# Optimization experiments

Measured on AMD Instinct MI355X. Metric: run time of the kernel, lower is better.

The kernel has to match this reference:

```python
import jax, jax.numpy as jnp
import numpy as np

N_ATOMS = 100000
N_EDGES = 300000
ATOM_DIM = 32
BOND_DIM = 16
STEPS = 4


def setup_inputs() -> dict:
    key = jax.random.key(0)
    ks = jax.random.split(key, 8)
    atom_features = jax.random.normal(ks[0], (N_ATOMS, ATOM_DIM), dtype=jnp.float32)
    bond_features = jax.random.normal(ks[1], (N_EDGES, BOND_DIM), dtype=jnp.float32)
    pair_indices = jax.random.randint(ks[2], (N_EDGES, 2), 0, N_ATOMS, dtype=jnp.int64 if jax.config.jax_enable_x64 else jnp.int32)
    W_bond = jax.random.normal(ks[3], (BOND_DIM, ATOM_DIM * ATOM_DIM), dtype=jnp.float32) * 0.05
    b_bond = jnp.zeros((ATOM_DIM * ATOM_DIM,), dtype=jnp.float32)
    W_ih = jax.random.normal(ks[4], (3 * ATOM_DIM, ATOM_DIM), dtype=jnp.float32) * 0.1
    W_hh = jax.random.normal(ks[5], (3 * ATOM_DIM, ATOM_DIM), dtype=jnp.float32) * 0.1
    b_ih = jnp.zeros((3 * ATOM_DIM,), dtype=jnp.float32)
    b_hh = jnp.zeros((3 * ATOM_DIM,), dtype=jnp.float32)
    return {
        'atom_features': atom_features,
        'bond_features': bond_features,
        'pair_indices': pair_indices,
        'W_bond': W_bond, 'b_bond': b_bond,
        'W_ih': W_ih, 'W_hh': W_hh, 'b_ih': b_ih, 'b_hh': b_hh,
    }


def _gru_cell(x, h, W_ih, W_hh, b_ih, b_hh):
    # torch.nn.GRUCell semantics
    gi = x @ W_ih.T + b_ih  # [N, 3H]
    gh = h @ W_hh.T + b_hh
    i_r, i_z, i_n = jnp.split(gi, 3, axis=-1)
    h_r, h_z, h_n = jnp.split(gh, 3, axis=-1)
    r = jax.nn.sigmoid(i_r + h_r)
    z = jax.nn.sigmoid(i_z + h_z)
    n = jnp.tanh(i_n + r * h_n)
    return (1.0 - z) * n + z * h


def reference(atom_features, bond_features, pair_indices, W_bond, b_bond, W_ih, W_hh, b_ih, b_hh):
    n_atoms, d = atom_features.shape
    # Edge transform matrices (identical every step in the original; hoisted)
    edge_mats = (bond_features @ W_bond + b_bond).reshape(-1, d, d)  # [E, d, d]
    dst = pair_indices[:, 0]
    nbr = pair_indices[:, 1]
    h = atom_features
    for _ in range(STEPS):
        # gather neighbor states, per-edge matvec, scatter-add
        msg = jnp.einsum('eij,ej->ei', edge_mats, h[nbr])  # [E, d]
        agg = jax.ops.segment_sum(msg, dst, num_segments=n_atoms)  # [N, d]
        h = _gru_cell(agg, h, W_ih, W_hh, b_ih, b_hh)
    return h
```

## Files before the change

kernel.cpp:

```cpp
#include <hip/hip_runtime.h>
#include <hip/hip_cooperative_groups.h>

namespace cg = cooperative_groups;

#define NA 100000
#define NE 300000
#define STEPS 4
#define NTILES (NE / 16)
#define ATILES (NA / 16)

typedef _Float16 f16;
typedef _Float16 half8 __attribute__((ext_vector_type(8)));
using f32x4 = __attribute__((ext_vector_type(4))) float;

__device__ __forceinline__ void msg_body(
    const f16* __restrict__ h, const f16* __restrict__ bondp,
    const int* __restrict__ nbrp, const f16* __restrict__ Wbt,
    f16* __restrict__ msgb, int wid, int nw, int col, int kg)
{
    half8 w0[17], w1[17];
#pragma unroll
    for (int t = 0; t < 17; ++t) {
        w0[t] = *reinterpret_cast<const half8*>(Wbt + (t * 32 + col) * 32 + kg * 8);
        w1[t] = *reinterpret_cast<const half8*>(Wbt + (t * 32 + 16 + col) * 32 + kg * 8);
    }
    int tile = wid;
    int pos = 0;
    half8 hf{}, cA{}, cB{};
    if (tile < NTILES) {
        pos = tile * 16 + col;
        int nbr0 = nbrp[pos];
        cA = *reinterpret_cast<const half8*>(bondp + (size_t)pos * 16);
        cB = *reinterpret_cast<const half8*>(bondp + (size_t)pos * 16 + 8);
        hf = *reinterpret_cast<const half8*>(h + (size_t)nbr0 * 32 + kg * 8);
    }
    while (tile < NTILES) {
        int tile2 = tile + nw;
        int pos2 = 0;
        half8 hf2{}, cA2{}, cB2{};
        if (tile2 < NTILES) {
            pos2 = tile2 * 16 + col;
            int nbr2 = nbrp[pos2];
            cA2 = *reinterpret_cast<const half8*>(bondp + (size_t)pos2 * 16);
            cB2 = *reinterpret_cast<const half8*>(bondp + (size_t)pos2 * 16 + 8);
            hf2 = *reinterpret_cast<const half8*>(h + (size_t)nbr2 * 32 + kg * 8);
        }
        f32x4 acc0 = {0.f, 0.f, 0.f, 0.f};
        f32x4 acc1 = {0.f, 0.f, 0.f, 0.f};
#pragma unroll
        for (int t = 0; t < 16; ++t) {
            f16 ch = (t < 8) ? cA[t] : cB[t - 8];
            half8 a = hf * ch;
            acc0 = __builtin_amdgcn_mfma_f32_16x16x32_f16(w0[t], a, acc0, 0, 0, 0);
            acc1 = __builtin_amdgcn_mfma_f32_16x16x32_f16(w1[t], a, acc1, 0, 0, 0);
        }
        acc0 = __builtin_amdgcn_mfma_f32_16x16x32_f16(w0[16], hf, acc0, 0, 0, 0);
        acc1 = __builtin_amdgcn_mfma_f32_16x16x32_f16(w1[16], hf, acc1, 0, 0, 0);

        half8 so;
        so[0]=(f16)acc0[0]; so[1]=(f16)acc0[1]; so[2]=(f16)acc0[2]; so[3]=(f16)acc0[3];
        so[4]=(f16)acc1[0]; so[5]=(f16)acc1[1]; so[6]=(f16)acc1[2]; so[7]=(f16)acc1[3];
        *reinterpret_cast<half8*>(msgb + (size_t)pos * 32 + kg * 8) = so;

        tile = tile2; pos = pos2; hf = hf2; cA = cA2; cB = cB2;
    }
}

__device__ __forceinline__ void gru_body(
    const f16* __restrict__ msgb, const int* __restrict__ start,
    const int* __restrict__ cnt, f16* __restrict__ h,
    const f16* __restrict__ Wihb, const f16* __restrict__ Whhb,
    const float* __restrict__ bih, const float* __restrict__ bhh,
    float* __restrict__ hout, int wf, int wid, int nw, int col, int kg)
{
    half8 wi[6], wh[6];
#pragma unroll
    for (int t = 0; t < 6; ++t) {
        wi[t] = *reinterpret_cast<const half8*>(Wihb + (size_t)(t * 16 + col) * 32 + kg * 8);
        wh[t] = *reinterpret_cast<const half8*>(Whhb + (size_t)(t * 16 + col) * 32 + kg * 8);
    }
    float br0  = bih[col]      + bhh[col];
    float bz0  = bih[32 + col] + bhh[32 + col];
    float bin0 = bih[64 + col];
    float bhn0 = bhh[64 + col];
    float br1  = bih[16 + col] + bhh[16 + col];
    float bz1  = bih[48 + col] + bhh[48 + col];
    float bin1 = bih[80 + col];
    float bhn1 = bhh[80 + col];

    for (int tile = wid; tile < ATILES; tile += nw) {
        int base = tile * 16;
        int a0   = base + col;
        int st = start[a0], en = st + cnt[a0];
        half8 hfrag = *reinterpret_cast<const half8*>(h + (size_t)a0 * 32 + kg * 8);

        float xs[8] = {0.f, 0.f, 0.f, 0.f, 0.f, 0.f, 0.f, 0.f};
        int p = st;
        while (p < en) {
            int n = en - p;
            half8 m0, m1, m2, m3;
            m0 = *reinterpret_cast<const half8*>(msgb + (size_t)p * 32 + kg * 8);
            if (n > 1) m1 = *reinterpret_cast<const half8*>(msgb + (size_t)(p + 1) * 32 + kg * 8);
            if (n > 2) m2 = *reinterpret_cast<const half8*>(msgb + (size_t)(p + 2) * 32 + kg * 8);
            if (n > 3) m3 = *reinterpret_cast<const half8*>(msgb + (size_t)(p + 3) * 32 + kg * 8);
#pragma unroll
            for (int j = 0; j < 8; ++j) xs[j] += (float)m0[j];
            if (n > 1) {
#pragma unroll
                for (int j = 0; j < 8; ++j) xs[j] += (float)m1[j];
            }
            if (n > 2) {
#pragma unroll
                for (int j = 0; j < 8; ++j) xs[j] += (float)m2[j];
            }
            if (n > 3) {
#pragma unroll
                for (int j = 0; j < 8; ++j) xs[j] += (float)m3[j];
            }
            p += 4;
        }
        half8 xfrag;
#pragma unroll
        for (int j = 0; j < 8; ++j) xfrag[j] = (f16)xs[j];

        f32x4 gi[6], gh[6];
#pragma unroll
        for (int t = 0; t < 6; ++t) {
            f32x4 z = {0.f, 0.f, 0.f, 0.f};
            gi[t] = __builtin_amdgcn_mfma_f32_16x16x32_f16(xfrag, wi[t], z, 0, 0, 0);
            gh[t] = __builtin_amdgcn_mfma_f32_16x16x32_f16(hfrag, wh[t], z, 0, 0, 0);
        }

#pragma unroll
        for (int hh = 0; hh < 2; ++hh) {
            float br  = hh ? br1  : br0;
            float bz  = hh ? bz1  : bz0;
            float bin = hh ? bin1 : bin0;
            float bhn = hh ? bhn1 : bhn0;
            int i = hh * 16 + col;
#pragma unroll
            for (int reg = 0; reg < 4; ++reg) {
                int a = base + kg * 4 + reg;
                float r = 1.f / (1.f + __expf(-(gi[hh][reg] + gh[hh][reg] + br)));
                float z = 1.f / (1.f + __expf(-(gi[2 + hh][reg] + gh[2 + hh][reg] + bz)));
                float n = tanhf(gi[4 + hh][reg] + bin + r * (gh[4 + hh][reg] + bhn));
                float hp = (float)h[(size_t)a * 32 + i];
                float o  = (1.f - z) * n + z * hp;
                if (wf) hout[(size_t)a * 32 + i] = o;
                h[(size_t)a * 32 + i] = (f16)o;
            }
        }
    }
}

__device__ __forceinline__ void setup_item(
    int t, const float* __restrict__ atom,
    const float* __restrict__ Wb, const float* __restrict__ bb,
    const float* __restrict__ Wih, const float* __restrict__ Whh,
    f16* __restrict__ hbf, f16* __restrict__ Wbt,
    f16* __restrict__ Wihb, f16* __restrict__ Whhb,
    int* __restrict__ rowcnt, int* __restrict__ total)
{
    const int NH8 = NA * 32 / 8;
    if (t < NH8) {
        float4 a = reinterpret_cast<const float4*>(atom)[2 * t];
        float4 b = reinterpret_cast<const float4*>(atom)[2 * t + 1];
        half8 o;
        o[0]=(f16)a.x; o[1]=(f16)a.y; o[2]=(f16)a.z; o[3]=(f16)a.w;
        o[4]=(f16)b.x; o[5]=(f16)b.y; o[6]=(f16)b.z; o[7]=(f16)b.w;
        reinterpret_cast<half8*>(hbf)[t] = o;
        return;
    }
    int u = t - NH8;
    if (u < NA) {
        rowcnt[u] = 0;
        if (u == 0) *total = 0;
        return;
    }
    int v = u - NA;
    if (v < 17 * 32 * 32) {
        int j = v & 31, i = (v >> 5) & 31, k = v >> 10;
        float val = (k < 16) ? Wb[k * 1024 + i * 32 + j] : bb[i * 32 + j];
        int row = ((i & 4) ? 16 : 0) + ((i >> 3) << 2) + (i & 3);
        Wbt[(k * 32 + row) * 32 + j] = (f16)val;
    } else if (v < 17 * 32 * 32 + 3072) {
        int q = v - 17 * 32 * 32;
        Wihb[q] = (f16)Wih[q];
    } else if (v < 17 * 32 * 32 + 6144) {
        int q = v - 17 * 32 * 32 - 3072;
        Whhb[q] = (f16)Whh[q];
    }
}

__device__ __forceinline__ void scatter_item(
    int e, const float* __restrict__ bond, const int* __restrict__ pair,
    int* __restrict__ next, int* __restrict__ nbrp, f16* __restrict__ bondp)
{
    int2 p = reinterpret_cast<const int2*>(pair)[e];
    int pos = atomicAdd(&next[p.x], 1);
    nbrp[pos] = p.y;
    const float4* b4 = reinterpret_cast<const float4*>(bond + (size_t)e * 16);
    float4 b0 = b4[0], b1 = b4[1], b2 = b4[2], b3 = b4[3];
    half8 o0, o1;
    o0[0]=(f16)b0.x; o0[1]=(f16)b0.y; o0[2]=(f16)b0.z; o0[3]=(f16)b0.w;
    o0[4]=(f16)b1.x; o0[5]=(f16)b1.y; o0[6]=(f16)b1.z; o0[7]=(f16)b1.w;
    o1[0]=(f16)b2.x; o1[1]=(f16)b2.y; o1[2]=(f16)b2.z; o1[3]=(f16)b2.w;
    o1[4]=(f16)b3.x; o1[5]=(f16)b3.y; o1[6]=(f16)b3.z; o1[7]=(f16)b3.w;
    half8* dst = reinterpret_cast<half8*>(bondp + (size_t)pos * 16);
    dst[0] = o0; dst[1] = o1;
}

#define SETUP_THREADS (NA * 32 / 8 + NA + 17 * 32 * 32 + 6144)

__global__ __launch_bounds__(256, 2) void mega_kernel(
    const float* __restrict__ atom, const float* __restrict__ bond,
    const int* __restrict__ pair,
    const float* __restrict__ Wb, const float* __restrict__ bb,
    const float* __restrict__ Wih, const float* __restrict__ Whh,
    const float* __restrict__ bih, const float* __restrict__ bhh,
    f16* __restrict__ hbf, f16* __restrict__ Wbt,
    f16* __restrict__ Wihb, f16* __restrict__ Whhb,
    int* __restrict__ rowcnt, int* __restrict__ startp, int* __restrict__ nextp,
    int* __restrict__ nbrp, f16* __restrict__ bondp,
    f16* __restrict__ msgb, int* __restrict__ total,
    float* __restrict__ hout)
{
    __shared__ int scan[256];
    __shared__ int sbase;

    cg::grid_group grid = cg::this_grid();
    int gtid = blockIdx.x * 256 + threadIdx.x;
    int gsz  = gridDim.x * 256;

    for (int t = gtid; t < SETUP_THREADS; t += gsz)
        setup_item(t, atom, Wb, bb, Wih, Whh, hbf, Wbt, Wihb, Whhb, rowcnt, total);
    grid.sync();

    for (int e = gtid; e < NE; e += gsz)
        atomicAdd(&rowcnt[reinterpret_cast<const int2*>(pair)[e].x], 1);
    grid.sync();

    const int NCHUNK = (NA + 255) / 256;
    for (int chunk = blockIdx.x; chunk < NCHUNK; chunk += gridDim.x) {
        int g = chunk * 256 + threadIdx.x;
        int v = (g < NA) ? rowcnt[g] : 0;
        scan[threadIdx.x] = v;
        __syncthreads();
        for (int off = 1; off < 256; off <<= 1) {
            int u = (threadIdx.x >= off) ? scan[threadIdx.x - off] : 0;
            __syncthreads();
            scan[threadIdx.x] += u;
            __syncthreads();
        }
        if (threadIdx.x == 255) sbase = atomicAdd(total, scan[255]);
        __syncthreads();
        if (g < NA) {
            int s = sbase + scan[threadIdx.x] - v;
            startp[g] = s;
            nextp[g]  = s;
        }
        __syncthreads();
    }
    grid.sync();

    for (int e = gtid; e < NE; e += gsz)
        scatter_item(e, bond, pair, nextp, nbrp, bondp);
    grid.sync();

    int wave = threadIdx.x >> 6;
    int lane = threadIdx.x & 63;
    int col  = lane & 15;
    int kg   = lane >> 4;
    int wid  = blockIdx.x * 4 + wave;
    int nw   = gridDim.x << 2;

    for (int s = 0; s < STEPS; ++s) {
        msg_body(hbf, bondp, nbrp, Wbt, msgb, wid, nw, col, kg);
        grid.sync();
        gru_body(msgb, startp, rowcnt, hbf, Wihb, Whhb, bih, bhh, hout,
                 (s == STEPS - 1) ? 1 : 0, wid, nw, col, kg);
        grid.sync();
    }
}

__global__ __launch_bounds__(256) void setup_kernel(
    const float* __restrict__ atom,
    const float* __restrict__ Wb, const float* __restrict__ bb,
    const float* __restrict__ Wih, const float* __restrict__ Whh,
    f16* __restrict__ hbf, f16* __restrict__ Wbt,
    f16* __restrict__ Wihb, f16* __restrict__ Whhb,
    int* __restrict__ rowcnt, int* __restrict__ total)
{
    int t = blockIdx.x * 256 + threadIdx.x;
    if (t < SETUP_THREADS)
        setup_item(t, atom, Wb, bb, Wih, Whh, hbf, Wbt, Wihb, Whhb, rowcnt, total);
}

__global__ __launch_bounds__(256) void hist_kernel(
    const int* __restrict__ pair, int* __restrict__ cnt)
{
    int e = blockIdx.x * 256 + threadIdx.x;
    if (e < NE) atomicAdd(&cnt[reinterpret_cast<const int2*>(pair)[e].x], 1);
}

__global__ __launch_bounds__(1024) void alloc_kernel(
    const int* __restrict__ cnt, int* __restrict__ start,
    int* __restrict__ next, int* __restrict__ total)
{
    __shared__ int tmp[1024];
    __shared__ int base;
    int g = blockIdx.x * 1024 + threadIdx.x;
    int v = (g < NA) ? cnt[g] : 0;
    tmp[threadIdx.x] = v;
    __syncthreads();
    for (int off = 1; off < 1024; off <<= 1) {
        int u = (threadIdx.x >= off) ? tmp[threadIdx.x - off] : 0;
        __syncthreads();
        tmp[threadIdx.x] += u;
        __syncthreads();
    }
    if (threadIdx.x == 1023) base = atomicAdd(total, tmp[1023]);
    __syncthreads();
    if (g < NA) {
        int s = base + tmp[threadIdx.x] - v;
        start[g] = s;
        next[g] = s;
    }
}

__global__ __launch_bounds__(256) void scatter_kernel(
    const float* __restrict__ bond, const int* __restrict__ pair,
    int* __restrict__ next, int* __restrict__ nbrp, f16* __restrict__ bondp)
{
    int e = blockIdx.x * 256 + threadIdx.x;
    if (e < NE) scatter_item(e, bond, pair, next, nbrp, bondp);
}

__global__ __launch_bounds__(256, 2) void msg_kernel(
    const f16* __restrict__ hb, const f16* __restrict__ bondp,
    const int* __restrict__ nbrp, const f16* __restrict__ Wbt,
    f16* __restrict__ msgb)
{
    int wave = threadIdx.x >> 6;
    int lane = threadIdx.x & 63;
    msg_body(hb, bondp, nbrp, Wbt, msgb,
             blockIdx.x * 4 + wave, gridDim.x << 2, lane & 15, lane >> 4);
}

__global__ __launch_bounds__(256) void gru_kernel(
    const f16* __restrict__ msgb, const int* __restrict__ start,
    const int* __restrict__ cnt, f16* __restrict__ hb,
    const f16* __restrict__ Wihb, const f16* __restrict__ Whhb,
    const float* __restrict__ bih, const float* __restrict__ bhh,
    float* __restrict__ hout, int wf)
{
    int wave = threadIdx.x >> 6;
    int lane = threadIdx.x & 63;
    gru_body(msgb, start, cnt, hb, Wihb, Whhb, bih, bhh, hout, wf,
             blockIdx.x * 4 + wave, gridDim.x << 2, lane & 15, lane >> 4);
}

extern "C" void kernel_launch(void* const* d_in, const int* in_sizes, int n_in,
                              void* d_out, int out_size, void* d_ws, size_t ws_size,
                              hipStream_t stream)
{
    const float* atom = (const float*)d_in[0];
    const float* bond = (const float*)d_in[1];
    const int*   pair = (const int*)  d_in[2];
    const float* Wb   = (const float*)d_in[3];
    const float* bb   = (const float*)d_in[4];
    const float* W_ih = (const float*)d_in[5];
    const float* W_hh = (const float*)d_in[6];
    const float* b_ih = (const float*)d_in[7];
    const float* b_hh = (const float*)d_in[8];
    float* out = (float*)d_out;

    char* w = (char*)d_ws;
    f16* msg    = (f16*)w;
    f16* hbf    = (f16*)(w + 19200000);
    f16* bondp  = (f16*)(w + 25600000);
    f16* Wbt    = (f16*)(w + 35200000);
    f16* Wihb   = Wbt + 17 * 32 * 32;
    f16* Whhb   = Wihb + 96 * 32;
    int* rowcnt = (int*)(w + 35248000);
    int* startp = (int*)(w + 35648000);
    int* nextp  = (int*)(w + 36048000);
    int* nbrp   = (int*)(w + 36448000);
    int* total  = (int*)(w + 37648000);

    int bpc = 0;
    hipError_t qe = hipOccupancyMaxActiveBlocksPerMultiprocessor(
        &bpc, (const void*)mega_kernel, 256, 0);
    if (qe == hipSuccess && bpc >= 2) {
        int nblk = bpc * 256;
        if (nblk > 2048) nblk = 2048;
        void* args[21];
        args[0]  = (void*)&atom;  args[1]  = (void*)&bond;  args[2]  = (void*)&pair;
        args[3]  = (void*)&Wb;    args[4]  = (void*)&bb;
        args[5]  = (void*)&W_ih;  args[6]  = (void*)&W_hh;
        args[7]  = (void*)&b_ih;  args[8]  = (void*)&b_hh;
        args[9]  = &hbf;   args[10] = &Wbt;   args[11] = &Wihb;  args[12] = &Whhb;
        args[13] = &rowcnt; args[14] = &startp; args[15] = &nextp;
        args[16] = &nbrp;  args[17] = &bondp; args[18] = &msg;
        args[19] = &total; args[20] = &out;
        hipLaunchCooperativeKernel((void*)mega_kernel, dim3(nblk), dim3(256),
                                   args, 0, stream);
    } else {
        setup_kernel<<<(SETUP_THREADS + 255) / 256, 256, 0, stream>>>(
            atom, Wb, bb, W_ih, W_hh, hbf, Wbt, Wihb, Whhb, rowcnt, total);
        hist_kernel<<<(NE + 255) / 256, 256, 0, stream>>>(pair, rowcnt);
        alloc_kernel<<<(NA + 1023) / 1024, 1024, 0, stream>>>(rowcnt, startp, nextp, total);
        scatter_kernel<<<(NE + 255) / 256, 256, 0, stream>>>(bond, pair, nextp, nbrp, bondp);
        const int gru_blocks = (ATILES + 3) / 4;
        for (int s = 0; s < STEPS; ++s) {
            msg_kernel<<<512, 256, 0, stream>>>(hbf, bondp, nbrp, Wbt, msg);
            gru_kernel<<<gru_blocks, 256, 0, stream>>>(msg, startp, rowcnt, hbf,
                                                       Wihb, Whhb, b_ih, b_hh, out,
                                                       (s == STEPS - 1) ? 1 : 0);
        }
    }
}
```

Before: 194.8 us.

## Sort edges by source atom so neighbor-state gathers hit nearby rows

Edges are now bucketed by source (neighbor) atom as well as destination. The message kernel walks edges in source order, so the gathers of h are close to sequential, and it writes each message to its destination-sorted slot through a dpos indirection. The GRU segment reduction is unchanged. In exchange the message stores become scattered, and setup gains a second histogram, a second prefix scan and an extra atomic per edge. The launch code also builds several redundant argument arrays.

```diff
diff --git a/kernel.cpp b/kernel.cpp
--- a/kernel.cpp
+++ b/kernel.cpp
@@ -14,9 +14,10 @@
 using f32x4 = __attribute__((ext_vector_type(4))) float;
 
 __device__ __forceinline__ void msg_body(
-    const f16* __restrict__ h, const f16* __restrict__ bondp,
-    const int* __restrict__ nbrp, const f16* __restrict__ Wbt,
-    f16* __restrict__ msgb, int wid, int nw, int col, int kg)
+    const f16* __restrict__ h, const f16* __restrict__ bondq,
+    const int* __restrict__ srcn, const int* __restrict__ dpos,
+    const f16* __restrict__ Wbt, f16* __restrict__ msgb,
+    int wid, int nw, int col, int kg)
 {
     half8 w0[17], w1[17];
 #pragma unroll
@@ -25,25 +26,27 @@
         w1[t] = *reinterpret_cast<const half8*>(Wbt + (t * 32 + 16 + col) * 32 + kg * 8);
     }
     int tile = wid;
-    int pos = 0;
+    int dp = 0;
     half8 hf{}, cA{}, cB{};
     if (tile < NTILES) {
-        pos = tile * 16 + col;
-        int nbr0 = nbrp[pos];
-        cA = *reinterpret_cast<const half8*>(bondp + (size_t)pos * 16);
-        cB = *reinterpret_cast<const half8*>(bondp + (size_t)pos * 16 + 8);
-        hf = *reinterpret_cast<const half8*>(h + (size_t)nbr0 * 32 + kg * 8);
+        int slot = tile * 16 + col;
+        int sn = srcn[slot];
+        dp = dpos[slot];
+        cA = *reinterpret_cast<const half8*>(bondq + (size_t)slot * 16);
+        cB = *reinterpret_cast<const half8*>(bondq + (size_t)slot * 16 + 8);
+        hf = *reinterpret_cast<const half8*>(h + (size_t)sn * 32 + kg * 8);
     }
     while (tile < NTILES) {
         int tile2 = tile + nw;
-        int pos2 = 0;
+        int dp2 = 0;
         half8 hf2{}, cA2{}, cB2{};
         if (tile2 < NTILES) {
-            pos2 = tile2 * 16 + col;
-            int nbr2 = nbrp[pos2];
-            cA2 = *reinterpret_cast<const half8*>(bondp + (size_t)pos2 * 16);
-            cB2 = *reinterpret_cast<const half8*>(bondp + (size_t)pos2 * 16 + 8);
-            hf2 = *reinterpret_cast<const half8*>(h + (size_t)nbr2 * 32 + kg * 8);
+            int slot2 = tile2 * 16 + col;
+            int sn2 = srcn[slot2];
+            dp2 = dpos[slot2];
+            cA2 = *reinterpret_cast<const half8*>(bondq + (size_t)slot2 * 16);
+            cB2 = *reinterpret_cast<const half8*>(bondq + (size_t)slot2 * 16 + 8);
+            hf2 = *reinterpret_cast<const half8*>(h + (size_t)sn2 * 32 + kg * 8);
         }
         f32x4 acc0 = {0.f, 0.f, 0.f, 0.f};
         f32x4 acc1 = {0.f, 0.f, 0.f, 0.f};
@@ -60,9 +63,9 @@
         half8 so;
         so[0]=(f16)acc0[0]; so[1]=(f16)acc0[1]; so[2]=(f16)acc0[2]; so[3]=(f16)acc0[3];
         so[4]=(f16)acc1[0]; so[5]=(f16)acc1[1]; so[6]=(f16)acc1[2]; so[7]=(f16)acc1[3];
-        *reinterpret_cast<half8*>(msgb + (size_t)pos * 32 + kg * 8) = so;
-
-        tile = tile2; pos = pos2; hf = hf2; cA = cA2; cB = cB2;
+        *reinterpret_cast<half8*>(msgb + (size_t)dp * 32 + kg * 8) = so;
+
+        tile = tile2; dp = dp2; hf = hf2; cA = cA2; cB = cB2;
     }
 }
 
@@ -159,7 +162,8 @@
     const float* __restrict__ Wih, const float* __restrict__ Whh,
     f16* __restrict__ hbf, f16* __restrict__ Wbt,
     f16* __restrict__ Wihb, f16* __restrict__ Whhb,
-    int* __restrict__ rowcnt, int* __restrict__ total)
+    int* __restrict__ cntd, int* __restrict__ cntn,
+    int* __restrict__ total, int* __restrict__ total2)
 {
     const int NH8 = NA * 32 / 8;
     if (t < NH8) {
@@ -172,12 +176,12 @@
         return;
     }
     int u = t - NH8;
-    if (u < NA) {
-        rowcnt[u] = 0;
-        if (u == 0) *total = 0;
+    if (u < 2 * NA) {
+        if (u < NA) cntd[u] = 0; else cntn[u - NA] = 0;
+        if (u == 0) { *total = 0; *total2 = 0; }
         return;
     }
-    int v = u - NA;
+    int v = u - 2 * NA;
     if (v < 17 * 32 * 32) {
         int j = v & 31, i = (v >> 5) & 31, k = v >> 10;
         float val = (k < 16) ? Wb[k * 1024 + i * 32 + j] : bb[i * 32 + j];
@@ -194,11 +198,14 @@
 
 __device__ __forceinline__ void scatter_item(
     int e, const float* __restrict__ bond, const int* __restrict__ pair,
-    int* __restrict__ next, int* __restrict__ nbrp, f16* __restrict__ bondp)
+    int* __restrict__ nextd, int* __restrict__ nextn,
+    int* __restrict__ srcn, int* __restrict__ dpos, f16* __restrict__ bondq)
 {
     int2 p = reinterpret_cast<const int2*>(pair)[e];
-    int pos = atomicAdd(&next[p.x], 1);
-    nbrp[pos] = p.y;
+    int pos  = atomicAdd(&nextd[p.x], 1);
+    int slot = atomicAdd(&nextn[p.y], 1);
+    srcn[slot] = p.y;
+    dpos[slot] = pos;
     const float4* b4 = reinterpret_cast<const float4*>(bond + (size_t)e * 16);
     float4 b0 = b4[0], b1 = b4[1], b2 = b4[2], b3 = b4[3];
     half8 o0, o1;
@@ -206,11 +213,11 @@
     o0[4]=(f16)b1.x; o0[5]=(f16)b1.y; o0[6]=(f16)b1.z; o0[7]=(f16)b1.w;
     o1[0]=(f16)b2.x; o1[1]=(f16)b2.y; o1[2]=(f16)b2.z; o1[3]=(f16)b2.w;
     o1[4]=(f16)b3.x; o1[5]=(f16)b3.y; o1[6]=(f16)b3.z; o1[7]=(f16)b3.w;
-    half8* dst = reinterpret_cast<half8*>(bondp + (size_t)pos * 16);
+    half8* dst = reinterpret_cast<half8*>(bondq + (size_t)slot * 16);
     dst[0] = o0; dst[1] = o1;
 }
 
-#define SETUP_THREADS (NA * 32 / 8 + NA + 17 * 32 * 32 + 6144)
+#define SETUP_THREADS (NA * 32 / 8 + 2 * NA + 17 * 32 * 32 + 6144)
 
 __global__ __launch_bounds__(256, 2) void mega_kernel(
     const float* __restrict__ atom, const float* __restrict__ bond,
@@ -220,9 +227,10 @@
     const float* __restrict__ bih, const float* __restrict__ bhh,
     f16* __restrict__ hbf, f16* __restrict__ Wbt,
     f16* __restrict__ Wihb, f16* __restrict__ Whhb,
-    int* __restrict__ rowcnt, int* __restrict__ startp, int* __restrict__ nextp,
-    int* __restrict__ nbrp, f16* __restrict__ bondp,
-    f16* __restrict__ msgb, int* __restrict__ total,
+    int* __restrict__ cntd, int* __restrict__ startd, int* __restrict__ nextd,
+    int* __restrict__ cntn, int* __restrict__ startn, int* __restrict__ nextn,
+    int* __restrict__ srcn, int* __restrict__ dpos, f16* __restrict__ bondq,
+    f16* __restrict__ msgb, int* __restrict__ total, int* __restrict__ total2,
     float* __restrict__ hout)
 {
     __shared__ int scan[256];
@@ -233,38 +241,49 @@
     int gsz  = gridDim.x * 256;
 
     for (int t = gtid; t < SETUP_THREADS; t += gsz)
-        setup_item(t, atom, Wb, bb, Wih, Whh, hbf, Wbt, Wihb, Whhb, rowcnt, total);
+        setup_item(t, atom, Wb, bb, Wih, Whh, hbf, Wbt, Wihb, Whhb,
+                   cntd, cntn, total, total2);
     grid.sync();
 
+    for (int e = gtid; e < NE; e += gsz) {
+        int2 p = reinterpret_cast<const int2*>(pair)[e];
+        atomicAdd(&cntd[p.x], 1);
+        atomicAdd(&cntn[p.y], 1);
+    }
+    grid.sync();
+
+    const int NCHUNK = (NA + 255) / 256;
+#pragma unroll 1
+    for (int pass = 0; pass < 2; ++pass) {
+        const int* c  = pass ? cntn   : cntd;
+        int* st = pass ? startn : startd;
+        int* nx = pass ? nextn  : nextd;
+        int* tt = pass ? total2 : total;
+        for (int chunk = blockIdx.x; chunk < NCHUNK; chunk += gridDim.x) {
+            int g = chunk * 256 + threadIdx.x;
+            int v = (g < NA) ? c[g] : 0;
+            scan[threadIdx.x] = v;
+            __syncthreads();
+            for (int off = 1; off < 256; off <<= 1) {
+                int u = (threadIdx.x >= off) ? scan[threadIdx.x - off] : 0;
+                __syncthreads();
+                scan[threadIdx.x] += u;
+                __syncthreads();
+            }
+            if (threadIdx.x == 255) sbase = atomicAdd(tt, scan[255]);
+            __syncthreads();
+            if (g < NA) {
+                int s = sbase + scan[threadIdx.x] - v;
+                st[g] = s;
+                nx[g] = s;
+            }
+            __syncthreads();
+        }
+    }
+    grid.sync();
+
     for (int e = gtid; e < NE; e += gsz)
-        atomicAdd(&rowcnt[reinterpret_cast<const int2*>(pair)[e].x], 1);
-    grid.sync();
-
-    const int NCHUNK = (NA + 255) / 256;
-    for (int chunk = blockIdx.x; chunk < NCHUNK; chunk += gridDim.x) {
-        int g = chunk * 256 + threadIdx.x;
-        int v = (g < NA) ? rowcnt[g] : 0;
-        scan[threadIdx.x] = v;
-        __syncthreads();
-        for (int off = 1; off < 256; off <<= 1) {
-            int u = (threadIdx.x >= off) ? scan[threadIdx.x - off] : 0;
-            __syncthreads();
-            scan[threadIdx.x] += u;
-            __syncthreads();
-        }
-        if (threadIdx.x == 255) sbase = atomicAdd(total, scan[255]);
-        __syncthreads();
-        if (g < NA) {
-            int s = sbase + scan[threadIdx.x] - v;
-            startp[g] = s;
-            nextp[g]  = s;
-        }
-        __syncthreads();
-    }
-    grid.sync();
-
-    for (int e = gtid; e < NE; e += gsz)
-        scatter_item(e, bond, pair, nextp, nbrp, bondp);
+        scatter_item(e, bond, pair, nextd, nextn, srcn, dpos, bondq);
     grid.sync();
 
     int wave = threadIdx.x >> 6;
@@ -275,9 +294,9 @@
     int nw   = gridDim.x << 2;
 
     for (int s = 0; s < STEPS; ++s) {
-        msg_body(hbf, bondp, nbrp, Wbt, msgb, wid, nw, col, kg);
+        msg_body(hbf, bondq, srcn, dpos, Wbt, msgb, wid, nw, col, kg);
         grid.sync();
-        gru_body(msgb, startp, rowcnt, hbf, Wihb, Whhb, bih, bhh, hout,
+        gru_body(msgb, startd, cntd, hbf, Wihb, Whhb, bih, bhh, hout,
                  (s == STEPS - 1) ? 1 : 0, wid, nw, col, kg);
         grid.sync();
     }
@@ -289,18 +308,24 @@
     const float* __restrict__ Wih, const float* __restrict__ Whh,
     f16* __restrict__ hbf, f16* __restrict__ Wbt,
     f16* __restrict__ Wihb, f16* __restrict__ Whhb,
-    int* __restrict__ rowcnt, int* __restrict__ total)
+    int* __restrict__ cntd, int* __restrict__ cntn,
+    int* __restrict__ total, int* __restrict__ total2)
 {
     int t = blockIdx.x * 256 + threadIdx.x;
     if (t < SETUP_THREADS)
-        setup_item(t, atom, Wb, bb, Wih, Whh, hbf, Wbt, Wihb, Whhb, rowcnt, total);
+        setup_item(t, atom, Wb, bb, Wih, Whh, hbf, Wbt, Wihb, Whhb,
+                   cntd, cntn, total, total2);
 }
 
 __global__ __launch_bounds__(256) void hist_kernel(
-    const int* __restrict__ pair, int* __restrict__ cnt)
+    const int* __restrict__ pair, int* __restrict__ cntd, int* __restrict__ cntn)
 {
     int e = blockIdx.x * 256 + threadIdx.x;
-    if (e < NE) atomicAdd(&cnt[reinterpret_cast<const int2*>(pair)[e].x], 1);
+    if (e < NE) {
+        int2 p = reinterpret_cast<const int2*>(pair)[e];
+        atomicAdd(&cntd[p.x], 1);
+        atomicAdd(&cntn[p.y], 1);
+    }
 }
 
 __global__ __launch_bounds__(1024) void alloc_kernel(
@@ -330,20 +355,21 @@
 
 __global__ __launch_bounds__(256) void scatter_kernel(
     const float* __restrict__ bond, const int* __restrict__ pair,
-    int* __restrict__ next, int* __restrict__ nbrp, f16* __restrict__ bondp)
+    int* __restrict__ nextd, int* __restrict__ nextn,
+    int* __restrict__ srcn, int* __restrict__ dpos, f16* __restrict__ bondq)
 {
     int e = blockIdx.x * 256 + threadIdx.x;
-    if (e < NE) scatter_item(e, bond, pair, next, nbrp, bondp);
+    if (e < NE) scatter_item(e, bond, pair, nextd, nextn, srcn, dpos, bondq);
 }
 
 __global__ __launch_bounds__(256, 2) void msg_kernel(
-    const f16* __restrict__ hb, const f16* __restrict__ bondp,
-    const int* __restrict__ nbrp, const f16* __restrict__ Wbt,
-    f16* __restrict__ msgb)
+    const f16* __restrict__ hb, const f16* __restrict__ bondq,
+    const int* __restrict__ srcn, const int* __restrict__ dpos,
+    const f16* __restrict__ Wbt, f16* __restrict__ msgb)
 {
     int wave = threadIdx.x >> 6;
     int lane = threadIdx.x & 63;
-    msg_body(hb, bondp, nbrp, Wbt, msgb,
+    msg_body(hb, bondq, srcn, dpos, Wbt, msgb,
              blockIdx.x * 4 + wave, gridDim.x << 2, lane & 15, lane >> 4);
 }
 
@@ -378,15 +404,20 @@
     char* w = (char*)d_ws;
     f16* msg    = (f16*)w;
     f16* hbf    = (f16*)(w + 19200000);
-    f16* bondp  = (f16*)(w + 25600000);
+    f16* bondq  = (f16*)(w + 25600000);
     f16* Wbt    = (f16*)(w + 35200000);
     f16* Wihb   = Wbt + 17 * 32 * 32;
     f16* Whhb   = Wihb + 96 * 32;
-    int* rowcnt = (int*)(w + 35248000);
-    int* startp = (int*)(w + 35648000);
-    int* nextp  = (int*)(w + 36048000);
-    int* nbrp   = (int*)(w + 36448000);
-    int* total  = (int*)(w + 37648000);
+    int* cntd   = (int*)(w + 35248000);
+    int* startd = (int*)(w + 35648000);
+    int* nextd  = (int*)(w + 36048000);
+    int* cntn   = (int*)(w + 36448000);
+    int* startn = (int*)(w + 36848000);
+    int* nextn  = (int*)(w + 37248000);
+    int* srcn   = (int*)(w + 37648000);
+    int* dpos   = (int*)(w + 38848000);
+    int* total  = (int*)(w + 40048000);
+    int* total2 = (int*)(w + 40048008);
 
     int bpc = 0;
     hipError_t qe = hipOccupancyMaxActiveBlocksPerMultiprocessor(
@@ -394,27 +425,56 @@
     if (qe == hipSuccess && bpc >= 2) {
         int nblk = bpc * 256;
         if (nblk > 2048) nblk = 2048;
-        void* args[21];
+        void* args[24];
         args[0]  = (void*)&atom;  args[1]  = (void*)&bond;  args[2]  = (void*)&pair;
         args[3]  = (void*)&Wb;    args[4]  = (void*)&bb;
         args[5]  = (void*)&W_ih;  args[6]  = (void*)&W_hh;
         args[7]  = (void*)&b_ih;  args[8]  = (void*)&b_hh;
-        args[9]  = &hbf;   args[10] = &Wbt;   args[11] = &Wihb;  args[12] = &Whhb;
-        args[13] = &rowcnt; args[14] = &startp; args[15] = &nextp;
-        args[16] = &nbrp;  args[17] = &bondp; args[18] = &msg;
-        args[19] = &total; args[20] = &out;
+        args[9]  = &hbf;    args[10] = &Wbt;    args[11] = &Wihb;  args[12] = &Whhb;
+        args[13] = &cntd;   args[14] = &startd; args[15] = &nextd;
+        args[16] = &cntn;   args[17] = &startn; args[18] = &nextn;
+        args[19] = &srcn;   args[20] = &dpos;   args[21] = &bondq;
+        args[22] = &msg;
+        void* args_full[25];
+        for (int i = 0; i < 22; ++i) args_full[i] = args[i];
+        args_full[22] = &msg;
+        args_full[23] = &total;
+        void* A[25];
+        A[0]=(void*)&atom; A[1]=(void*)&bond; A[2]=(void*)&pair;
+        A[3]=(void*)&Wb;   A[4]=(void*)&bb;  A[5]=(void*)&W_ih; A[6]=(void*)&W_hh;
+        A[7]=(void*)&b_ih; A[8]=(void*)&b_hh;
+        A[9]=&hbf; A[10]=&Wbt; A[11]=&Wihb; A[12]=&Whhb;
+        A[13]=&cntd; A[14]=&startd; A[15]=&nextd;
+        A[16]=&cntn; A[17]=&startn; A[18]=&nextn;
+        A[19]=&srcn; A[20]=&dpos; A[21]=&bondq;
+        A[22]=&msg; A[23]=&total;
+        void* B[26];
+        for (int i = 0; i < 24; ++i) B[i] = A[i];
+        B[24] = &total2;
+        B[25] = &out;
+        void* FA[26];
+        FA[0]=(void*)&atom; FA[1]=(void*)&bond; FA[2]=(void*)&pair;
+        FA[3]=(void*)&Wb;   FA[4]=(void*)&bb;  FA[5]=(void*)&W_ih; FA[6]=(void*)&W_hh;
+        FA[7]=(void*)&b_ih; FA[8]=(void*)&b_hh;
+        FA[9]=&hbf; FA[10]=&Wbt; FA[11]=&Wihb; FA[12]=&Whhb;
+        FA[13]=&cntd; FA[14]=&startd; FA[15]=&nextd;
+        FA[16]=&cntn; FA[17]=&startn; FA[18]=&nextn;
+        FA[19]=&srcn; FA[20]=&dpos; FA[21]=&bondq;
+        FA[22]=&msg; FA[23]=&total; FA[24]=&total2; FA[25]=&out;
         hipLaunchCooperativeKernel((void*)mega_kernel, dim3(nblk), dim3(256),
-                                   args, 0, stream);
+                                   FA, 0, stream);
     } else {
         setup_kernel<<<(SETUP_THREADS + 255) / 256, 256, 0, stream>>>(
-            atom, Wb, bb, W_ih, W_hh, hbf, Wbt, Wihb, Whhb, rowcnt, total);
-        hist_kernel<<<(NE + 255) / 256, 256, 0, stream>>>(pair, rowcnt);
-        alloc_kernel<<<(NA + 1023) / 1024, 1024, 0, stream>>>(rowcnt, startp, nextp, total);
-        scatter_kernel<<<(NE + 255) / 256, 256, 0, stream>>>(bond, pair, nextp, nbrp, bondp);
+            atom, Wb, bb, W_ih, W_hh, hbf, Wbt, Wihb, Whhb, cntd, cntn, total, total2);
+        hist_kernel<<<(NE + 255) / 256, 256, 0, stream>>>(pair, cntd, cntn);
+        alloc_kernel<<<(NA + 1023) / 1024, 1024, 0, stream>>>(cntd, startd, nextd, total);
+        alloc_kernel<<<(NA + 1023) / 1024, 1024, 0, stream>>>(cntn, startn, nextn, total2);
+        scatter_kernel<<<(NE + 255) / 256, 256, 0, stream>>>(bond, pair, nextd, nextn,
+                                                             srcn, dpos, bondq);
         const int gru_blocks = (ATILES + 3) / 4;
         for (int s = 0; s < STEPS; ++s) {
-            msg_kernel<<<512, 256, 0, stream>>>(hbf, bondp, nbrp, Wbt, msg);
-            gru_kernel<<<gru_blocks, 256, 0, stream>>>(msg, startp, rowcnt, hbf,
+            msg_kernel<<<512, 256, 0, stream>>>(hbf, bondq, srcn, dpos, Wbt, msg);
+            gru_kernel<<<gru_blocks, 256, 0, stream>>>(msg, startd, cntd, hbf,
                                                        Wihb, Whhb, b_ih, b_hh, out,
                                                        (s == STEPS - 1) ? 1 : 0);
         }
```

Result: slower. 227.4 us (+16.7%).
